# Kernel optimization log

Hardware: AMD Instinct MI355X
Metric: run time of the kernel (lower is better)

The kernel has to match this reference:

```python
import jax, jax.numpy as jnp
import numpy as np

B = 64          # batch
T = 12000       # signal length
P = 50          # patch size
D = 200         # embed dim
L = 12          # depth
H = 10          # heads
HD = D // H     # head dim = 20
FF = 4 * D      # mlp hidden = 800
N = T // P      # 240 patches
S = N + 1       # seq len with cls token
NRD = (2 * N - 1) * 1 + 3   # 482 relative distances (window (240,1))
NC = 1000       # classes
SCALE = HD ** -0.5
EPS = 1e-6


def _rel_index():
    # static [S,S] int index into the relative-position-bias table (window (N,1))
    w0, w1 = N, 1
    coords = np.stack(np.meshgrid(np.arange(w0), np.arange(w1), indexing='ij'))
    cf = coords.reshape(2, -1)                      # [2, N]
    rc = (cf[:, :, None] - cf[:, None, :]).transpose(1, 2, 0).copy()
    rc[:, :, 0] += w0 - 1
    rc[:, :, 1] += w1 - 1
    rc[:, :, 0] *= 2 * w1 - 1
    idx = np.zeros((w0 * w1 + 1,) * 2, dtype=np.int32)
    idx[1:, 1:] = rc.sum(-1)
    idx[0, :] = NRD - 3
    idx[:, 0] = NRD - 2
    idx[0, 0] = NRD - 1
    return idx

REL_IDX = jnp.asarray(_rel_index())


def _ln(x, s, b):
    m = x.mean(-1, keepdims=True)
    v = ((x - m) ** 2).mean(-1, keepdims=True)
    return (x - m) * jax.lax.rsqrt(v + EPS) * s + b


def setup_inputs() -> dict:
    key = jax.random.key(0)
    ks = jax.random.split(key, 12)
    nrm = lambda k, shp, std=0.02: jax.random.normal(k, shp, jnp.float32) * std
    return {
        'x': jax.random.normal(ks[0], (B, 1, T), jnp.float32),
        'conv_w': nrm(ks[1], (D, 1, P)),
        'conv_b': jnp.zeros((D,), jnp.float32),
        'cls_token': nrm(ks[2], (1, 1, D)),
        'pos_embed': nrm(ks[3], (1, S, D)),
        'ln1_s': jnp.ones((L, D), jnp.float32), 'ln1_b': jnp.zeros((L, D), jnp.float32),
        'qkv_w': nrm(ks[4], (L, 3 * D, D)),
        'q_bias': jnp.zeros((L, D), jnp.float32), 'v_bias': jnp.zeros((L, D), jnp.float32),
        'rpb_table': nrm(ks[5], (L, NRD, H)),
        'proj_w': nrm(ks[6], (L, D, D)), 'proj_b': jnp.zeros((L, D), jnp.float32),
        'ln2_s': jnp.ones((L, D), jnp.float32), 'ln2_b': jnp.zeros((L, D), jnp.float32),
        'fc1_w': nrm(ks[7], (L, FF, D)), 'fc1_b': jnp.zeros((L, FF), jnp.float32),
        'fc2_w': nrm(ks[8], (L, D, FF)), 'fc2_b': jnp.zeros((L, D), jnp.float32),
        'fc_norm_s': jnp.ones((D,), jnp.float32), 'fc_norm_b': jnp.zeros((D,), jnp.float32),
        'head_w': nrm(ks[9], (NC, D)), 'head_b': jnp.zeros((NC,), jnp.float32),
    }


def reference(x, conv_w, conv_b, cls_token, pos_embed,
              ln1_s, ln1_b, qkv_w, q_bias, v_bias, rpb_table, proj_w, proj_b,
              ln2_s, ln2_b, fc1_w, fc1_b, fc2_w, fc2_b,
              fc_norm_s, fc_norm_b, head_w, head_b):
    b = x.shape[0]
    # PatchEmbed: Conv1d with stride == kernel -> reshape + GEMM
    patches = x[:, 0].reshape(b, N, P)                       # [B,N,P]
    tok = patches @ conv_w[:, 0].T + conv_b                   # [B,N,D]
    tok = jnp.concatenate([jnp.broadcast_to(cls_token, (b, 1, D)), tok], axis=1)
    tok = tok + pos_embed                                     # [B,S,D]

    for i in range(L):
        h = _ln(tok, ln1_s[i], ln1_b[i])
        qkv_bias = jnp.concatenate([q_bias[i], jnp.zeros_like(v_bias[i]), v_bias[i]])
        qkv = (h @ qkv_w[i].T + qkv_bias).reshape(b, S, 3, H, HD)
        qkv = qkv.transpose(2, 0, 3, 1, 4)                    # [3,B,H,S,HD]
        q, k, v = qkv[0], qkv[1], qkv[2]
        attn = jnp.einsum('bhqd,bhkd->bhqk', q * SCALE, k)    # [B,H,S,S]
        bias = rpb_table[i][REL_IDX]                          # [S,S,H]
        attn = jax.nn.softmax(attn + bias.transpose(2, 0, 1)[None], axis=-1)
        o = jnp.einsum('bhqk,bhkd->bqhd', attn, v).reshape(b, S, D)
        tok = tok + o @ proj_w[i].T + proj_b[i]
        h2 = _ln(tok, ln2_s[i], ln2_b[i])
        h2 = jax.nn.gelu(h2 @ fc1_w[i].T + fc1_b[i], approximate=False)
        tok = tok + h2 @ fc2_w[i].T + fc2_b[i]

    pooled = _ln(tok[:, 1:].mean(axis=1), fc_norm_s, fc_norm_b)   # mean pooling over patch tokens
    return pooled @ head_w.T + head_b                             # [B, NC]
```

## Files before the change

### kernel.cpp

```cpp
#include <hip/hip_runtime.h>
#include <math.h>

#define Bz 64
#define Tz 12000
#define Pz 50
#define Dz 200
#define Lz 12
#define Hz 10
#define HDz 20
#define FFz 800
#define Nz 240
#define Sz 241
#define Sp 256
#define NRDz 482
#define NCz 1000
#define BS (Bz * Sz)
#define Mp (Bz * Sp)
#define Kp 224
#define PEM (Bz * Nz)
#define SCALEq 0.22360679774997896f
#define LOG2E 1.4426950408889634f
#define SCALE2f (SCALEq * LOG2E)
#define BIASL 655360

typedef __attribute__((ext_vector_type(8))) short bf16x8;
typedef __attribute__((ext_vector_type(4))) float f32x4;

static __device__ __forceinline__ short f2b(float f) {
    unsigned u = __float_as_uint(f);
    unsigned r = (u + 0x7fffu + ((u >> 16) & 1u)) >> 16;
    return (short)r;
}
static __device__ __forceinline__ float b2f(short v) {
    return __uint_as_float(((unsigned)(unsigned short)v) << 16);
}
static __device__ __forceinline__ uint2 pk4(float a, float b, float c, float d) {
    uint2 r;
    asm("v_cvt_pk_bf16_f32 %0, %1, %2" : "=v"(r.x) : "v"(a), "v"(b));
    asm("v_cvt_pk_bf16_f32 %0, %1, %2" : "=v"(r.y) : "v"(c), "v"(d));
    return r;
}
static __device__ __forceinline__ float frcp(float x) {
    float r;
    asm("v_rcp_f32 %0, %1" : "=v"(r) : "v"(x));
    return r;
}
static __device__ __forceinline__ float gelu_f(float v) {
    float u = v * (0.7978845608f + 0.03567740814f * v * v);
    float e = exp2f(2.885390082f * u);
    return v * e * frcp(e + 1.f);
}
static __device__ __forceinline__ void gll16(const void* g, void* l) {
    __builtin_amdgcn_global_load_lds((const __attribute__((address_space(1))) unsigned*)g,
                                     (__attribute__((address_space(3))) unsigned*)l, 16, 0, 0);
}
template <int N> static __device__ __forceinline__ void wait_vm() {
    if constexpr (N == 0) asm volatile("s_waitcnt vmcnt(0)" ::: "memory");
    else if constexpr (N == 1) asm volatile("s_waitcnt vmcnt(1)" ::: "memory");
    else if constexpr (N == 2) asm volatile("s_waitcnt vmcnt(2)" ::: "memory");
    else if constexpr (N == 3) asm volatile("s_waitcnt vmcnt(3)" ::: "memory");
    else if constexpr (N == 4) asm volatile("s_waitcnt vmcnt(4)" ::: "memory");
    else if constexpr (N == 5) asm volatile("s_waitcnt vmcnt(5)" ::: "memory");
    else if constexpr (N == 6) asm volatile("s_waitcnt vmcnt(6)" ::: "memory");
}

__global__ void cvt_pad_k(const float* __restrict__ in, short* __restrict__ out,
                          int N, int K, int Npad, int Kpad, int total) {
    int i = blockIdx.x * 256 + threadIdx.x;
    if (i >= total) return;
    int pk = Npad * Kpad;
    int l = i / pk;
    int r = i - l * pk;
    int n = r / Kpad;
    int k = r - n * Kpad;
    float v = (n < N && k < K) ? in[((size_t)l * N + n) * K + k] : 0.f;
    out[i] = f2b(v);
}

__global__ void xcvt_k(const float* __restrict__ x, short* __restrict__ xb) {
    int i = blockIdx.x * 256 + threadIdx.x;
    int m = i >> 6, k = i & 63;
    int b = m / Nz, j = m - b * Nz;
    xb[i] = (k < Pz) ? f2b(x[(size_t)b * Tz + j * Pz + k]) : 0;
}

__global__ void cls_k(const float* __restrict__ cls, const float* __restrict__ pos,
                      float* __restrict__ tok) {
    int b = blockIdx.x, d = threadIdx.x;
    if (d < Dz) tok[(size_t)b * Sp * Dz + d] = cls[d] + pos[d];
}

__global__ void ln_k(const float* __restrict__ in, short* __restrict__ out,
                     const float* __restrict__ sc, const float* __restrict__ bi) {
    int wave = threadIdx.x >> 6, lane = threadIdx.x & 63;
    int row = blockIdx.x * 4 + wave;
    if ((row & 255) >= Sz) return;
    const float* x = in + (size_t)row * Dz;
    float v[4];
    float sum = 0.f;
    #pragma unroll
    for (int i = 0; i < 4; ++i) {
        int d = lane + 64 * i;
        v[i] = (d < Dz) ? x[d] : 0.f;
        sum += v[i];
    }
    #pragma unroll
    for (int off = 32; off; off >>= 1) sum += __shfl_xor(sum, off);
    float mean = sum * (1.f / Dz);
    float var = 0.f;
    #pragma unroll
    for (int i = 0; i < 4; ++i) {
        int d = lane + 64 * i;
        if (d < Dz) { float t = v[i] - mean; var += t * t; }
    }
    #pragma unroll
    for (int off = 32; off; off >>= 1) var += __shfl_xor(var, off);
    var *= (1.f / Dz);
    float rstd = rsqrtf(var + 1e-6f);
    short* o = out + (size_t)row * Kp;
    #pragma unroll
    for (int i = 0; i < 4; ++i) {
        int d = lane + 64 * i;
        if (d < Dz) o[d] = f2b((v[i] - mean) * rstd * sc[d] + bi[d]);
        else if (d < Kp) o[d] = 0;
    }
}

__global__ void bias_pre4_k(const float* __restrict__ tabs, short* __restrict__ bp) {
    int l = blockIdx.y;
    int tid = blockIdx.x * 256 + threadIdx.x;
    const float* tab = tabs + (size_t)l * NRDz * Hz;
    int lane = tid & 63;
    int mi = (tid >> 6) & 1;
    int w  = (tid >> 7) & 3;
    int qb = (tid >> 9) & 1;
    int nj = (tid >> 10) & 3;
    int kc = (tid >> 12) & 3;
    int h  = tid >> 14;
    int q  = qb * 128 + w * 32 + mi * 16 + (lane & 15);
    int k0 = kc * 64 + nj * 16 + 4 * (lane >> 4);
    short4 o;
    #pragma unroll
    for (int r = 0; r < 4; ++r) {
        int k = k0 + r;
        float v;
        if (q > Nz || k > Nz) v = -1e30f;
        else if (k == 0)      v = (q == 0) ? tab[481 * Hz + h] : tab[480 * Hz + h];
        else if (q == 0)      v = tab[479 * Hz + h];
        else                  v = tab[(q - k + 239) * Hz + h];
        ((short*)&o)[r] = f2b(v * LOG2E);
    }
    *(short4*)(bp + (size_t)l * BIASL + (size_t)tid * 4) = o;
}

template <int MODE, int BN2, int BM2>
__global__ __launch_bounds__(256) void gemm8_k(
        const short* __restrict__ A, const short* __restrict__ W,
        const float* __restrict__ bias, const float* __restrict__ bias2,
        const float* __restrict__ res, void* __restrict__ outv,
        short* __restrict__ qo, short* __restrict__ ko, short* __restrict__ vo,
        int M, int Nreal, int K, int strideA, int ldo, int gridx, int gridy) {
    constexpr int NJ = BN2 / 32;
    constexpr int MI = BM2 / 32;
    constexpr int AISS = BM2 / 64;
    constexpr int BISS = BN2 / 64;
    constexpr int LPS = AISS + BISS;
    __shared__ short smem[3 * (BM2 + BN2) * 32];
    short* Asb = smem;
    short* Bsb = smem + 3 * BM2 * 32;
    const int t = threadIdx.x;
    const int lane = t & 63, w = t >> 6;
    const int l15 = lane & 15, lg = lane >> 4;
    const int wm = w & 1, wn = w >> 1;

    int bx, by;
    {
        int wg = blockIdx.x;
        if ((gridy & 7) == 0) {
            int xcd = wg & 7, j = wg >> 3;
            bx = j % gridx;
            by = (j / gridx) * 8 + xcd;
        } else {
            bx = wg % gridx;
            by = wg / gridx;
        }
    }
    const int row0 = by * BM2, col0 = bx * BN2;
    const int xsw = (l15 >> 1) & 3;

    f32x4 acc[MI][NJ];
    #pragma unroll
    for (int mi = 0; mi < MI; ++mi)
        #pragma unroll
        for (int nj = 0; nj < NJ; ++nj) {
            f32x4 z = {0.f, 0.f, 0.f, 0.f};
            acc[mi][nj] = z;
        }

    const int nk = K >> 5;

    auto stage = [&](int buf, int kt) {
        const int k0 = kt * 32;
        #pragma unroll
        for (int i = 0; i < AISS; ++i) {
            int c = (w * AISS + i) * 64 + lane;
            int r = c >> 2, q = c & 3;
            const short* gp = A + (size_t)(row0 + r) * strideA + k0 + ((q ^ ((r >> 1) & 3)) * 8);
            gll16(gp, Asb + buf * BM2 * 32 + (w * AISS + i) * 512);
        }
        #pragma unroll
        for (int i = 0; i < BISS; ++i) {
            int c = (w * BISS + i) * 64 + lane;
            int r = c >> 2, q = c & 3;
            const short* gp = W + (size_t)(col0 + r) * K + k0 + ((q ^ ((r >> 1) & 3)) * 8);
            gll16(gp, Bsb + buf * BN2 * 32 + (w * BISS + i) * 512);
        }
    };

    stage(0, 0);
    if (nk > 1) stage(1, 1);
    for (int kt = 0; kt < nk; ++kt) {
        const int cur = kt % 3;
        if (kt + 1 < nk) wait_vm<LPS>();
        else             wait_vm<0>();
        __builtin_amdgcn_s_barrier();
        if (kt + 2 < nk) stage((kt + 2) % 3, kt + 2);
        bf16x8 bfr[NJ], afr[MI];
        #pragma unroll
        for (int nj = 0; nj < NJ; ++nj)
            bfr[nj] = *(const bf16x8*)(Bsb + cur * BN2 * 32 + (wn * (BN2 / 2) + nj * 16 + l15) * 32 + ((lg ^ xsw) * 8));
        #pragma unroll
        for (int mi = 0; mi < MI; ++mi)
            afr[mi] = *(const bf16x8*)(Asb + cur * BM2 * 32 + (wm * (BM2 / 2) + mi * 16 + l15) * 32 + ((lg ^ xsw) * 8));
        #pragma unroll
        for (int mi = 0; mi < MI; ++mi)
            #pragma unroll
            for (int nj = 0; nj < NJ; ++nj) {
                if (MODE == 1)
                    acc[mi][nj] = __builtin_amdgcn_mfma_f32_16x16x32_bf16(bfr[nj], afr[mi], acc[mi][nj], 0, 0, 0);
                else
                    acc[mi][nj] = __builtin_amdgcn_mfma_f32_16x16x32_bf16(afr[mi], bfr[nj], acc[mi][nj], 0, 0, 0);
            }
    }

    if (MODE == 1) {
        #pragma unroll
        for (int mi = 0; mi < MI; ++mi) {
            int m = row0 + wm * (BM2 / 2) + mi * 16 + l15;
            int b = m >> 8, s = m & 255;
            #pragma unroll
            for (int nj = 0; nj < NJ; ++nj) {
                int n0 = col0 + wn * (BN2 / 2) + nj * 16 + 4 * lg;
                if (n0 >= 600) continue;
                int which = n0 >= 400 ? 2 : (n0 >= 200 ? 1 : 0);
                int hd = n0 - which * 200;
                int h = hd / 20, d0 = hd - h * 20;
                size_t base = (size_t)(b * Hz + h) * 8192;
                if (which == 0) {
                    f32x4 qb4 = *(const f32x4*)(bias + hd);
                    short4 o4;
                    #pragma unroll
                    for (int r = 0; r < 4; ++r)
                        ((short*)&o4)[r] = f2b((acc[mi][nj][r] + qb4[r]) * SCALE2f);
                    *(short4*)(qo + base + s * 32 + d0) = o4;
                } else if (which == 1) {
                    int oct = (d0 >> 3) ^ ((s >> 1) & 3);
                    short4 o4;
                    #pragma unroll
                    for (int r = 0; r < 4; ++r)
                        ((short*)&o4)[r] = f2b(acc[mi][nj][r]);
                    *(short4*)(ko + base + s * 32 + oct * 8 + (d0 & 7)) = o4;
                } else {
                    f32x4 vb4 = *(const f32x4*)(bias2 + hd);
                    #pragma unroll
                    for (int r = 0; r < 4; ++r) {
                        int d = d0 + r;
                        vo[base + d * 256 + (s ^ ((d & 7) << 3))] = f2b(acc[mi][nj][r] + vb4[r]);
                    }
                }
            }
        }
        return;
    }

    if (MODE == 2 || MODE == 3) {
        __syncthreads();
        if (MODE == 3) {
            constexpr int EW = BN2 + 8;
            short* ep = smem;
            #pragma unroll
            for (int mi = 0; mi < MI; ++mi)
                #pragma unroll
                for (int nj = 0; nj < NJ; ++nj) {
                    int nl = wn * (BN2 / 2) + nj * 16 + l15;
                    int n = col0 + nl;
                    float bv = (n < Nreal) ? bias[n] : 0.f;
                    #pragma unroll
                    for (int r = 0; r < 4; ++r)
                        ep[(wm * (BM2 / 2) + mi * 16 + 4 * lg + r) * EW + nl] =
                            f2b(gelu_f(acc[mi][nj][r] + bv));
                }
            __syncthreads();
            constexpr int TPR = BN2 / 8;
            constexpr int RPP = 256 / TPR;
            int rowp = t / TPR, cch = t % TPR;
            #pragma unroll
            for (int p = 0; p < BM2 / RPP; ++p) {
                int row = p * RPP + rowp;
                int n = col0 + cch * 8;
                if (n + 8 <= Nreal)
                    *(bf16x8*)((short*)outv + (size_t)(row0 + row) * ldo + n) =
                        *(const bf16x8*)(ep + row * EW + cch * 8);
            }
        } else {
            constexpr int EWF = BN2 + 4;
            float* epf = (float*)smem;
            #pragma unroll
            for (int mi = 0; mi < MI; ++mi)
                #pragma unroll
                for (int nj = 0; nj < NJ; ++nj) {
                    int nl = wn * (BN2 / 2) + nj * 16 + l15;
                    int n = col0 + nl;
                    float bv = (n < Nreal) ? bias[n] : 0.f;
                    #pragma unroll
                    for (int r = 0; r < 4; ++r)
                        epf[(wm * (BM2 / 2) + mi * 16 + 4 * lg + r) * EWF + nl] =
                            acc[mi][nj][r] + bv;
                }
            __syncthreads();
            constexpr int TPR = BN2 / 4;
            constexpr int RPP = 256 / TPR;
            int rowp = t / TPR, cch = t % TPR;
            #pragma unroll
            for (int p = 0; p < BM2 / RPP; ++p) {
                int row = p * RPP + rowp;
                int n = col0 + cch * 4;
                if (n + 4 <= Nreal) {
                    size_t off = (size_t)(row0 + row) * ldo + n;
                    f32x4 v = *(const f32x4*)(epf + row * EWF + cch * 4);
                    f32x4 rr = *(const f32x4*)(res + off);
                    *(f32x4*)((float*)outv + off) = v + rr;
                }
            }
        }
        return;
    }

    #pragma unroll
    for (int mi = 0; mi < MI; ++mi) {
        #pragma unroll
        for (int nj = 0; nj < NJ; ++nj) {
            int n = col0 + wn * (BN2 / 2) + nj * 16 + l15;
            if (n >= Nreal) continue;
            if (MODE == 4) {
                #pragma unroll
                for (int r = 0; r < 4; ++r) {
                    int m = row0 + wm * (BM2 / 2) + mi * 16 + 4 * lg + r;
                    int bb = m / Nz, j = m - bb * Nz;
                    size_t trow = (size_t)bb * Sp + j + 1;
                    ((float*)outv)[trow * ldo + n] =
                        acc[mi][nj][r] + bias[n] + res[(size_t)(j + 1) * Dz + n];
                }
            } else {
                #pragma unroll
                for (int r = 0; r < 4; ++r) {
                    int m = row0 + wm * (BM2 / 2) + mi * 16 + 4 * lg + r;
                    if (m >= M) continue;
                    size_t off = (size_t)m * ldo + n;
                    ((float*)outv)[off] = acc[mi][nj][r] + bias[n];
                }
            }
        }
    }
}

#define PLD 72
__global__ __launch_bounds__(256) void attn5_k(const short* __restrict__ Qb,
                                               const short* __restrict__ Kb,
                                               const short* __restrict__ Vtb,
                                               const short* __restrict__ biasC,
                                               short* __restrict__ o) {
    const int blk = blockIdx.x;
    const int qb = blk & 1;
    const int bh = blk >> 1;
    const int b = bh / Hz, h = bh - b * Hz;
    __shared__ short Ks[8192];
    __shared__ short Vt[8192];
    __shared__ short Pl[4][32 * PLD];
    const int t = threadIdx.x;
    const int lane = t & 63, w = t >> 6;
    const int l15 = lane & 15, lg = lane >> 4;

    const short* kbh = Kb + (size_t)bh * 8192;
    const short* vbh = Vtb + (size_t)bh * 8192;
    #pragma unroll
    for (int i = 0; i < 4; ++i) {
        int j = w * 4 + i;
        gll16(kbh + (size_t)(j * 64 + lane) * 8, Ks + j * 512);
        gll16(vbh + (size_t)(j * 64 + lane) * 8, Vt + j * 512);
    }
    bf16x8 qfrag[2];
    const short* qbh = Qb + (size_t)bh * 8192;
    #pragma unroll
    for (int mi = 0; mi < 2; ++mi) {
        int qrow = qb * 128 + w * 32 + mi * 16 + l15;
        qfrag[mi] = *(const bf16x8*)(qbh + qrow * 32 + lg * 8);
    }
    const short* bpp = biasC + 4 * (size_t)(lane + 128 * w + 512 * qb + 16384 * h);
    __syncthreads();

    f32x4 O[2][2];
    float mrow[2] = {-1e30f, -1e30f};
    float lrow[2] = {0.f, 0.f};
    {
        f32x4 z = {0.f, 0.f, 0.f, 0.f};
        O[0][0] = z; O[0][1] = z; O[1][0] = z; O[1][1] = z;
    }
    const int xsw = (l15 >> 1) & 3;

    #pragma unroll 1
    for (int kc = 0; kc < 4; ++kc) {
        bf16x8 kf[4];
        #pragma unroll
        for (int nj = 0; nj < 4; ++nj)
            kf[nj] = *(const bf16x8*)(Ks + (kc * 64 + nj * 16 + l15) * 32 + ((lg ^ xsw) * 8));
        f32x4 s[2][4];
        __builtin_amdgcn_s_setprio(1);
        #pragma unroll
        for (int mi = 0; mi < 2; ++mi)
            #pragma unroll
            for (int nj = 0; nj < 4; ++nj) {
                f32x4 z = {0.f, 0.f, 0.f, 0.f};
                s[mi][nj] = __builtin_amdgcn_mfma_f32_16x16x32_bf16(kf[nj], qfrag[mi], z, 0, 0, 0);
            }
        __builtin_amdgcn_s_setprio(0);
        const short* bkc = bpp + kc * 16384;
        #pragma unroll
        for (int mi = 0; mi < 2; ++mi)
            #pragma unroll
            for (int nj = 0; nj < 4; ++nj) {
                short4 bp4 = *(const short4*)(bkc + nj * 4096 + mi * 256);
                s[mi][nj][0] += b2f(bp4.x);
                s[mi][nj][1] += b2f(bp4.y);
                s[mi][nj][2] += b2f(bp4.z);
                s[mi][nj][3] += b2f(bp4.w);
            }
        #pragma unroll
        for (int mi = 0; mi < 2; ++mi) {
            float mx = s[mi][0][0];
            #pragma unroll
            for (int nj = 0; nj < 4; ++nj)
                #pragma unroll
                for (int c = 0; c < 4; ++c) mx = fmaxf(mx, s[mi][nj][c]);
            mx = fmaxf(mx, __shfl_xor(mx, 16));
            mx = fmaxf(mx, __shfl_xor(mx, 32));
            float ssum = 0.f;
            if (__all(mx - mrow[mi] <= 8.f)) {
                float mn = mrow[mi];
                #pragma unroll
                for (int nj = 0; nj < 4; ++nj)
                    #pragma unroll
                    for (int c = 0; c < 4; ++c) {
                        float p = exp2f(s[mi][nj][c] - mn);
                        s[mi][nj][c] = p;
                        ssum += p;
                    }
                ssum += __shfl_xor(ssum, 16);
                ssum += __shfl_xor(ssum, 32);
                lrow[mi] += ssum;
            } else {
                float mn = fmaxf(mrow[mi], mx);
                float scn = exp2f(mrow[mi] - mn);
                mrow[mi] = mn;
                #pragma unroll
                for (int nj = 0; nj < 4; ++nj)
                    #pragma unroll
                    for (int c = 0; c < 4; ++c) {
                        float p = exp2f(s[mi][nj][c] - mn);
                        s[mi][nj][c] = p;
                        ssum += p;
                    }
                ssum += __shfl_xor(ssum, 16);
                ssum += __shfl_xor(ssum, 32);
                lrow[mi] = lrow[mi] * scn + ssum;
                f32x4 scd;
                #pragma unroll
                for (int r = 0; r < 4; ++r) scd[r] = __shfl(scn, 4 * lg + r);
                O[mi][0] *= scd;
                O[mi][1] *= scd;
            }
            #pragma unroll
            for (int nj = 0; nj < 4; ++nj)
                *(uint2*)(Pl[w] + (mi * 16 + l15) * PLD + nj * 16 + 4 * lg) =
                    pk4(s[mi][nj][0], s[mi][nj][1], s[mi][nj][2], s[mi][nj][3]);
        }
        #pragma unroll
        for (int kk = 0; kk < 2; ++kk) {
            bf16x8 vf[2];
            #pragma unroll
            for (int dj = 0; dj < 2; ++dj) {
                int d = dj * 16 + l15;
                int cb = (kc * 128 + kk * 64 + lg * 16) ^ ((l15 & 7) << 4);
                vf[dj] = *(const bf16x8*)((const char*)Vt + d * 512 + cb);
            }
            __builtin_amdgcn_s_setprio(1);
            #pragma unroll
            for (int mi = 0; mi < 2; ++mi) {
                bf16x8 af = *(const bf16x8*)(Pl[w] + (mi * 16 + l15) * PLD + kk * 32 + lg * 8);
                O[mi][0] = __builtin_amdgcn_mfma_f32_16x16x32_bf16(af, vf[0], O[mi][0], 0, 0, 0);
                O[mi][1] = __builtin_amdgcn_mfma_f32_16x16x32_bf16(af, vf[1], O[mi][1], 0, 0, 0);
            }
            __builtin_amdgcn_s_setprio(0);
        }
    }

    #pragma unroll
    for (int mi = 0; mi < 2; ++mi) {
        float linv = 1.f / lrow[mi];
        f32x4 invd;
        #pragma unroll
        for (int r = 0; r < 4; ++r) invd[r] = __shfl(linv, 4 * lg + r);
        #pragma unroll
        for (int dj = 0; dj < 2; ++dj) {
            int d = dj * 16 + l15;
            if (d >= HDz) continue;
            #pragma unroll
            for (int r = 0; r < 4; ++r) {
                int q = qb * 128 + w * 32 + mi * 16 + 4 * lg + r;
                if (q < Sz)
                    o[((size_t)b * Sp + q) * Kp + h * HDz + d] = f2b(O[mi][dj][r] * invd[r]);
            }
        }
    }
}

__global__ void pool_norm_k(const float* __restrict__ tok, const float* __restrict__ sc,
                            const float* __restrict__ bi, short* __restrict__ pooled) {
    int b = blockIdx.x;
    int t = threadIdx.x;
    float val = 0.f;
    if (t < Dz) {
        const float* base = tok + ((size_t)b * Sp + 1) * Dz + t;
        float s = 0.f;
        for (int si = 0; si < Nz; ++si) s += base[(size_t)si * Dz];
        val = s * (1.f / Nz);
    }
    __shared__ float red[8];
    float sum = val, sq = val * val;
    #pragma unroll
    for (int off = 32; off; off >>= 1) { sum += __shfl_xor(sum, off); sq += __shfl_xor(sq, off); }
    int wave = t >> 6, lane = t & 63;
    if (lane == 0) { red[wave] = sum; red[4 + wave] = sq; }
    __syncthreads();
    sum = red[0] + red[1] + red[2] + red[3];
    sq = red[4] + red[5] + red[6] + red[7];
    float mean = sum * (1.f / Dz);
    float var = sq * (1.f / Dz) - mean * mean;
    float rstd = rsqrtf(var + 1e-6f);
    if (t < Dz) pooled[(size_t)b * Kp + t] = f2b((val - mean) * rstd * sc[t] + bi[t]);
    else if (t < Kp) pooled[(size_t)b * Kp + t] = 0;
}

extern "C" void kernel_launch(void* const* d_in, const int* in_sizes, int n_in,
                              void* d_out, int out_size, void* d_ws, size_t ws_size,
                              hipStream_t stream) {
    const float* x        = (const float*)d_in[0];
    const float* conv_w   = (const float*)d_in[1];
    const float* conv_b   = (const float*)d_in[2];
    const float* cls_tok  = (const float*)d_in[3];
    const float* pos_emb  = (const float*)d_in[4];
    const float* ln1_s    = (const float*)d_in[5];
    const float* ln1_b    = (const float*)d_in[6];
    const float* qkv_w    = (const float*)d_in[7];
    const float* q_bias   = (const float*)d_in[8];
    const float* v_bias   = (const float*)d_in[9];
    const float* rpb      = (const float*)d_in[10];
    const float* proj_w   = (const float*)d_in[11];
    const float* proj_b   = (const float*)d_in[12];
    const float* ln2_s    = (const float*)d_in[13];
    const float* ln2_b    = (const float*)d_in[14];
    const float* fc1_w    = (const float*)d_in[15];
    const float* fc1_b    = (const float*)d_in[16];
    const float* fc2_w    = (const float*)d_in[17];
    const float* fc2_b    = (const float*)d_in[18];
    const float* fcn_s    = (const float*)d_in[19];
    const float* fcn_b    = (const float*)d_in[20];
    const float* head_w   = (const float*)d_in[21];
    const float* head_b   = (const float*)d_in[22];
    float* out = (float*)d_out;

    char* ws = (char*)d_ws;
    float* tok  = (float*)ws;  ws += (size_t)Mp * Dz * 4;
    short* xa   = (short*)ws;  ws += (size_t)Mp * Kp * 2;
    short* xb   = (short*)ws;  ws += (size_t)Mp * Kp * 2;
    short* xc   = (short*)ws;  ws += (size_t)Mp * Kp * 2;
    short* mid  = (short*)ws;  ws += (size_t)Mp * FFz * 2;
    short* Qb   = (short*)ws;  ws += (size_t)640 * 8192 * 2;
    short* Kb   = (short*)ws;  ws += (size_t)640 * 8192 * 2;
    short* Vtb  = (short*)ws;  ws += (size_t)640 * 8192 * 2;
    short* wq = (short*)ws;    ws += (size_t)Lz * 640 * Kp * 2;
    short* wp = (short*)ws;    ws += (size_t)Lz * 256 * Kp * 2;
    short* w1 = (short*)ws;    ws += (size_t)Lz * 896 * Kp * 2;
    short* w2 = (short*)ws;    ws += (size_t)Lz * 256 * FFz * 2;
    short* wh = (short*)ws;    ws += (size_t)1024 * Kp * 2;
    short* biasC = (short*)ws; ws += (size_t)Lz * BIASL * 2;
    short* xpb  = (short*)ws;  ws += (size_t)PEM * 64 * 2;
    short* wpe  = (short*)ws;  ws += (size_t)256 * 64 * 2;
    short* pooledb = (short*)ws; ws += (size_t)128 * Kp * 2;

    hipMemsetAsync(xa, 0, (size_t)Mp * Kp * 2, stream);
    hipMemsetAsync(pooledb, 0, (size_t)128 * Kp * 2, stream);

    {
        int n;
        n = Lz * 640 * Kp;  cvt_pad_k<<<(n + 255) / 256, 256, 0, stream>>>(qkv_w, wq, 600, 200, 640, Kp, n);
        n = Lz * 256 * Kp;  cvt_pad_k<<<(n + 255) / 256, 256, 0, stream>>>(proj_w, wp, 200, 200, 256, Kp, n);
        n = Lz * 896 * Kp;  cvt_pad_k<<<(n + 255) / 256, 256, 0, stream>>>(fc1_w, w1, 800, 200, 896, Kp, n);
        n = Lz * 256 * FFz; cvt_pad_k<<<(n + 255) / 256, 256, 0, stream>>>(fc2_w, w2, 200, 800, 256, FFz, n);
        n = 1024 * Kp;      cvt_pad_k<<<(n + 255) / 256, 256, 0, stream>>>(head_w, wh, 1000, 200, 1024, Kp, n);
        n = 256 * 64;       cvt_pad_k<<<(n + 255) / 256, 256, 0, stream>>>(conv_w, wpe, 200, 50, 256, 64, n);
    }
    bias_pre4_k<<<dim3(640, Lz), 256, 0, stream>>>(rpb, biasC);

    xcvt_k<<<(PEM * 64) / 256, 256, 0, stream>>>(x, xpb);
    gemm8_k<4, 64, 128><<<4 * (PEM / 128), 256, 0, stream>>>(
        xpb, wpe, conv_b, nullptr, pos_emb, tok,
        nullptr, nullptr, nullptr, PEM, Dz, 64, 64, Dz, 4, PEM / 128);
    cls_k<<<Bz, 256, 0, stream>>>(cls_tok, pos_emb, tok);

    dim3 blk(256);
    ln_k<<<Mp / 4, blk, 0, stream>>>(tok, xa, ln1_s, ln1_b);
    for (int l = 0; l < Lz; ++l) {
        gemm8_k<1, 128, 64><<<5 * (Mp / 64), blk, 0, stream>>>(
            xa, wq + (size_t)l * 640 * Kp, q_bias + l * Dz, v_bias + l * Dz,
            nullptr, nullptr, Qb, Kb, Vtb,
            Mp, 600, Kp, Kp, 0, 5, Mp / 64);
        attn5_k<<<1280, blk, 0, stream>>>(Qb, Kb, Vtb, biasC + (size_t)l * BIASL, xb);
        gemm8_k<2, 64, 64><<<4 * (Mp / 64), blk, 0, stream>>>(
            xb, wp + (size_t)l * 256 * Kp, proj_b + l * Dz, nullptr,
            tok, tok, nullptr, nullptr, nullptr,
            Mp, Dz, Kp, Kp, Dz, 4, Mp / 64);
        ln_k<<<Mp / 4, blk, 0, stream>>>(tok, xc, ln2_s + l * Dz, ln2_b + l * Dz);
        gemm8_k<3, 128, 64><<<7 * (Mp / 64), blk, 0, stream>>>(
            xc, w1 + (size_t)l * 896 * Kp, fc1_b + l * FFz, nullptr,
            nullptr, mid, nullptr, nullptr, nullptr,
            Mp, FFz, Kp, Kp, FFz, 7, Mp / 64);
        gemm8_k<2, 64, 64><<<4 * (Mp / 64), blk, 0, stream>>>(
            mid, w2 + (size_t)l * 256 * FFz, fc2_b + l * Dz, nullptr,
            tok, tok, nullptr, nullptr, nullptr,
            Mp, Dz, FFz, FFz, Dz, 4, Mp / 64);
        ln_k<<<Mp / 4, blk, 0, stream>>>(tok, xa, ln1_s + (size_t)((l + 1) % Lz) * Dz,
                                         ln1_b + (size_t)((l + 1) % Lz) * Dz);
    }

    pool_norm_k<<<Bz, blk, 0, stream>>>(tok, fcn_s, fcn_b, pooledb);
    gemm8_k<0, 128, 128><<<8, blk, 0, stream>>>(
        pooledb, wh, head_b, nullptr, nullptr, out,
        nullptr, nullptr, nullptr, Bz, NCz, Kp, Kp, NCz, 8, 1);
}
```

Before: 1.355 ms.

## Process all query rows per (batch,head) block in attention; vectorize layernorm

The attention kernel now launches one block per (batch, head) instead of two, with each wave handling 64 query rows in two halves. This halves the redundant K/V loads into shared memory and is meant to reuse them across more queries. The bias precompute layout is changed to match the new indexing. LayerNorm switches to float4 loads and short4 stores. The cost is fewer blocks (640 on a large GPU), which lowers occupancy and parallelism, and more registers per wave.

```diff
diff --git a/kernel.cpp b/kernel.cpp
--- a/kernel.cpp
+++ b/kernel.cpp
@@ -96,48 +96,46 @@
     int row = blockIdx.x * 4 + wave;
     if ((row & 255) >= Sz) return;
     const float* x = in + (size_t)row * Dz;
-    float v[4];
-    float sum = 0.f;
-    #pragma unroll
-    for (int i = 0; i < 4; ++i) {
-        int d = lane + 64 * i;
-        v[i] = (d < Dz) ? x[d] : 0.f;
-        sum += v[i];
-    }
+    f32x4 v = {0.f, 0.f, 0.f, 0.f};
+    if (lane < 50) v = *(const f32x4*)(x + lane * 4);
+    float sum = v[0] + v[1] + v[2] + v[3];
     #pragma unroll
     for (int off = 32; off; off >>= 1) sum += __shfl_xor(sum, off);
     float mean = sum * (1.f / Dz);
     float var = 0.f;
-    #pragma unroll
-    for (int i = 0; i < 4; ++i) {
-        int d = lane + 64 * i;
-        if (d < Dz) { float t = v[i] - mean; var += t * t; }
+    if (lane < 50) {
+        #pragma unroll
+        for (int i = 0; i < 4; ++i) { float d = v[i] - mean; var += d * d; }
     }
     #pragma unroll
     for (int off = 32; off; off >>= 1) var += __shfl_xor(var, off);
-    var *= (1.f / Dz);
-    float rstd = rsqrtf(var + 1e-6f);
+    float rstd = rsqrtf(var * (1.f / Dz) + 1e-6f);
     short* o = out + (size_t)row * Kp;
-    #pragma unroll
-    for (int i = 0; i < 4; ++i) {
-        int d = lane + 64 * i;
-        if (d < Dz) o[d] = f2b((v[i] - mean) * rstd * sc[d] + bi[d]);
-        else if (d < Kp) o[d] = 0;
-    }
-}
-
-__global__ void bias_pre4_k(const float* __restrict__ tabs, short* __restrict__ bp) {
+    if (lane < 50) {
+        f32x4 s4 = *(const f32x4*)(sc + lane * 4);
+        f32x4 b4 = *(const f32x4*)(bi + lane * 4);
+        short4 o4;
+        #pragma unroll
+        for (int r = 0; r < 4; ++r)
+            ((short*)&o4)[r] = f2b((v[r] - mean) * rstd * s4[r] + b4[r]);
+        *(short4*)(o + lane * 4) = o4;
+    } else if (lane < 56) {
+        short4 z = {0, 0, 0, 0};
+        *(short4*)(o + lane * 4) = z;
+    }
+}
+
+__global__ void bias_pre5_k(const float* __restrict__ tabs, short* __restrict__ bp) {
     int l = blockIdx.y;
     int tid = blockIdx.x * 256 + threadIdx.x;
     const float* tab = tabs + (size_t)l * NRDz * Hz;
     int lane = tid & 63;
-    int mi = (tid >> 6) & 1;
-    int w  = (tid >> 7) & 3;
-    int qb = (tid >> 9) & 1;
+    int mi = (tid >> 6) & 3;
+    int w  = (tid >> 8) & 3;
     int nj = (tid >> 10) & 3;
     int kc = (tid >> 12) & 3;
     int h  = tid >> 14;
-    int q  = qb * 128 + w * 32 + mi * 16 + (lane & 15);
+    int q  = w * 64 + mi * 16 + (lane & 15);
     int k0 = kc * 64 + nj * 16 + 4 * (lane >> 4);
     short4 o;
     #pragma unroll
@@ -375,14 +373,12 @@
 }
 
 #define PLD 72
-__global__ __launch_bounds__(256) void attn5_k(const short* __restrict__ Qb,
+__global__ __launch_bounds__(256) void attn6_k(const short* __restrict__ Qb,
                                                const short* __restrict__ Kb,
                                                const short* __restrict__ Vtb,
                                                const short* __restrict__ biasC,
                                                short* __restrict__ o) {
-    const int blk = blockIdx.x;
-    const int qb = blk & 1;
-    const int bh = blk >> 1;
+    const int bh = blockIdx.x;
     const int b = bh / Hz, h = bh - b * Hz;
     __shared__ short Ks[8192];
     __shared__ short Vt[8192];
@@ -399,22 +395,23 @@
         gll16(kbh + (size_t)(j * 64 + lane) * 8, Ks + j * 512);
         gll16(vbh + (size_t)(j * 64 + lane) * 8, Vt + j * 512);
     }
-    bf16x8 qfrag[2];
+    bf16x8 qfrag[4];
     const short* qbh = Qb + (size_t)bh * 8192;
     #pragma unroll
-    for (int mi = 0; mi < 2; ++mi) {
-        int qrow = qb * 128 + w * 32 + mi * 16 + l15;
+    for (int mi = 0; mi < 4; ++mi) {
+        int qrow = w * 64 + mi * 16 + l15;
         qfrag[mi] = *(const bf16x8*)(qbh + qrow * 32 + lg * 8);
     }
-    const short* bpp = biasC + 4 * (size_t)(lane + 128 * w + 512 * qb + 16384 * h);
+    const short* bpp = biasC + 4 * (size_t)(lane + 256 * w + 16384 * h);
     __syncthreads();
 
-    f32x4 O[2][2];
-    float mrow[2] = {-1e30f, -1e30f};
-    float lrow[2] = {0.f, 0.f};
+    f32x4 O[4][2];
+    float mrow[4] = {-1e30f, -1e30f, -1e30f, -1e30f};
+    float lrow[4] = {0.f, 0.f, 0.f, 0.f};
     {
         f32x4 z = {0.f, 0.f, 0.f, 0.f};
-        O[0][0] = z; O[0][1] = z; O[1][0] = z; O[1][1] = z;
+        #pragma unroll
+        for (int mi = 0; mi < 4; ++mi) { O[mi][0] = z; O[mi][1] = z; }
     }
     const int xsw = (l15 >> 1) & 3;
 
@@ -424,98 +421,106 @@
         #pragma unroll
         for (int nj = 0; nj < 4; ++nj)
             kf[nj] = *(const bf16x8*)(Ks + (kc * 64 + nj * 16 + l15) * 32 + ((lg ^ xsw) * 8));
-        f32x4 s[2][4];
-        __builtin_amdgcn_s_setprio(1);
-        #pragma unroll
-        for (int mi = 0; mi < 2; ++mi)
-            #pragma unroll
-            for (int nj = 0; nj < 4; ++nj) {
-                f32x4 z = {0.f, 0.f, 0.f, 0.f};
-                s[mi][nj] = __builtin_amdgcn_mfma_f32_16x16x32_bf16(kf[nj], qfrag[mi], z, 0, 0, 0);
-            }
-        __builtin_amdgcn_s_setprio(0);
-        const short* bkc = bpp + kc * 16384;
-        #pragma unroll
-        for (int mi = 0; mi < 2; ++mi)
-            #pragma unroll
-            for (int nj = 0; nj < 4; ++nj) {
-                short4 bp4 = *(const short4*)(bkc + nj * 4096 + mi * 256);
-                s[mi][nj][0] += b2f(bp4.x);
-                s[mi][nj][1] += b2f(bp4.y);
-                s[mi][nj][2] += b2f(bp4.z);
-                s[mi][nj][3] += b2f(bp4.w);
-            }
-        #pragma unroll
-        for (int mi = 0; mi < 2; ++mi) {
-            float mx = s[mi][0][0];
-            #pragma unroll
-            for (int nj = 0; nj < 4; ++nj)
-                #pragma unroll
-                for (int c = 0; c < 4; ++c) mx = fmaxf(mx, s[mi][nj][c]);
-            mx = fmaxf(mx, __shfl_xor(mx, 16));
-            mx = fmaxf(mx, __shfl_xor(mx, 32));
-            float ssum = 0.f;
-            if (__all(mx - mrow[mi] <= 8.f)) {
-                float mn = mrow[mi];
+        #pragma unroll
+        for (int mih = 0; mih < 2; ++mih) {
+            f32x4 s[2][4];
+            __builtin_amdgcn_s_setprio(1);
+            #pragma unroll
+            for (int m2 = 0; m2 < 2; ++m2) {
+                int mi = mih * 2 + m2;
+                #pragma unroll
+                for (int nj = 0; nj < 4; ++nj) {
+                    f32x4 z = {0.f, 0.f, 0.f, 0.f};
+                    s[m2][nj] = __builtin_amdgcn_mfma_f32_16x16x32_bf16(kf[nj], qfrag[mi], z, 0, 0, 0);
+                }
+            }
+            __builtin_amdgcn_s_setprio(0);
+            #pragma unroll
+            for (int m2 = 0; m2 < 2; ++m2) {
+                int mi = mih * 2 + m2;
+                #pragma unroll
+                for (int nj = 0; nj < 4; ++nj) {
+                    short4 bp4 = *(const short4*)(bpp + 4 * (64 * mi + 1024 * nj + 4096 * kc));
+                    s[m2][nj][0] += b2f(bp4.x);
+                    s[m2][nj][1] += b2f(bp4.y);
+                    s[m2][nj][2] += b2f(bp4.z);
+                    s[m2][nj][3] += b2f(bp4.w);
+                }
+            }
+            #pragma unroll
+            for (int m2 = 0; m2 < 2; ++m2) {
+                int mi = mih * 2 + m2;
+                float mx = s[m2][0][0];
                 #pragma unroll
                 for (int nj = 0; nj < 4; ++nj)
                     #pragma unroll
-                    for (int c = 0; c < 4; ++c) {
-                        float p = exp2f(s[mi][nj][c] - mn);
-                        s[mi][nj][c] = p;
-                        ssum += p;
-                    }
-                ssum += __shfl_xor(ssum, 16);
-                ssum += __shfl_xor(ssum, 32);
-                lrow[mi] += ssum;
-            } else {
-                float mn = fmaxf(mrow[mi], mx);
-                float scn = exp2f(mrow[mi] - mn);
-                mrow[mi] = mn;
+                    for (int c = 0; c < 4; ++c) mx = fmaxf(mx, s[m2][nj][c]);
+                mx = fmaxf(mx, __shfl_xor(mx, 16));
+                mx = fmaxf(mx, __shfl_xor(mx, 32));
+                float ssum = 0.f;
+                if (__all(mx - mrow[mi] <= 8.f)) {
+                    float mn = mrow[mi];
+                    #pragma unroll
+                    for (int nj = 0; nj < 4; ++nj)
+                        #pragma unroll
+                        for (int c = 0; c < 4; ++c) {
+                            float p = exp2f(s[m2][nj][c] - mn);
+                            s[m2][nj][c] = p;
+                            ssum += p;
+                        }
+                    ssum += __shfl_xor(ssum, 16);
+                    ssum += __shfl_xor(ssum, 32);
+                    lrow[mi] += ssum;
+                } else {
+                    float mn = fmaxf(mrow[mi], mx);
+                    float scn = exp2f(mrow[mi] - mn);
+                    mrow[mi] = mn;
+                    #pragma unroll
+                    for (int nj = 0; nj < 4; ++nj)
+                        #pragma unroll
+                        for (int c = 0; c < 4; ++c) {
+                            float p = exp2f(s[m2][nj][c] - mn);
+                            s[m2][nj][c] = p;
+                            ssum += p;
+                        }
+                    ssum += __shfl_xor(ssum, 16);
+                    ssum += __shfl_xor(ssum, 32);
+                    lrow[mi] = lrow[mi] * scn + ssum;
+                    f32x4 scd;
+                    #pragma unroll
+                    for (int r = 0; r < 4; ++r) scd[r] = __shfl(scn, 4 * lg + r);
+                    O[mi][0] *= scd;
+                    O[mi][1] *= scd;
+                }
                 #pragma unroll
                 for (int nj = 0; nj < 4; ++nj)
-                    #pragma unroll
-                    for (int c = 0; c < 4; ++c) {
-                        float p = exp2f(s[mi][nj][c] - mn);
-                        s[mi][nj][c] = p;
-                        ssum += p;
-                    }
-                ssum += __shfl_xor(ssum, 16);
-                ssum += __shfl_xor(ssum, 32);
-                lrow[mi] = lrow[mi] * scn + ssum;
-                f32x4 scd;
-                #pragma unroll
-                for (int r = 0; r < 4; ++r) scd[r] = __shfl(scn, 4 * lg + r);
-                O[mi][0] *= scd;
-                O[mi][1] *= scd;
-            }
-            #pragma unroll
-            for (int nj = 0; nj < 4; ++nj)
-                *(uint2*)(Pl[w] + (mi * 16 + l15) * PLD + nj * 16 + 4 * lg) =
-                    pk4(s[mi][nj][0], s[mi][nj][1], s[mi][nj][2], s[mi][nj][3]);
-        }
-        #pragma unroll
-        for (int kk = 0; kk < 2; ++kk) {
-            bf16x8 vf[2];
-            #pragma unroll
-            for (int dj = 0; dj < 2; ++dj) {
-                int d = dj * 16 + l15;
-                int cb = (kc * 128 + kk * 64 + lg * 16) ^ ((l15 & 7) << 4);
-                vf[dj] = *(const bf16x8*)((const char*)Vt + d * 512 + cb);
-            }
-            __builtin_amdgcn_s_setprio(1);
-            #pragma unroll
-            for (int mi = 0; mi < 2; ++mi) {
-                bf16x8 af = *(const bf16x8*)(Pl[w] + (mi * 16 + l15) * PLD + kk * 32 + lg * 8);
-                O[mi][0] = __builtin_amdgcn_mfma_f32_16x16x32_bf16(af, vf[0], O[mi][0], 0, 0, 0);
-                O[mi][1] = __builtin_amdgcn_mfma_f32_16x16x32_bf16(af, vf[1], O[mi][1], 0, 0, 0);
-            }
-            __builtin_amdgcn_s_setprio(0);
-        }
-    }
-
-    #pragma unroll
-    for (int mi = 0; mi < 2; ++mi) {
+                    *(uint2*)(Pl[w] + (m2 * 16 + l15) * PLD + nj * 16 + 4 * lg) =
+                        pk4(s[m2][nj][0], s[m2][nj][1], s[m2][nj][2], s[m2][nj][3]);
+            }
+            #pragma unroll
+            for (int kk = 0; kk < 2; ++kk) {
+                bf16x8 vf[2];
+                #pragma unroll
+                for (int dj = 0; dj < 2; ++dj) {
+                    int d = dj * 16 + l15;
+                    int cb = (kc * 128 + kk * 64 + lg * 16) ^ ((l15 & 7) << 4);
+                    vf[dj] = *(const bf16x8*)((const char*)Vt + d * 512 + cb);
+                }
+                __builtin_amdgcn_s_setprio(1);
+                #pragma unroll
+                for (int m2 = 0; m2 < 2; ++m2) {
+                    int mi = mih * 2 + m2;
+                    bf16x8 af = *(const bf16x8*)(Pl[w] + (m2 * 16 + l15) * PLD + kk * 32 + lg * 8);
+                    O[mi][0] = __builtin_amdgcn_mfma_f32_16x16x32_bf16(af, vf[0], O[mi][0], 0, 0, 0);
+                    O[mi][1] = __builtin_amdgcn_mfma_f32_16x16x32_bf16(af, vf[1], O[mi][1], 0, 0, 0);
+                }
+                __builtin_amdgcn_s_setprio(0);
+            }
+        }
+    }
+
+    #pragma unroll
+    for (int mi = 0; mi < 4; ++mi) {
         float linv = 1.f / lrow[mi];
         f32x4 invd;
         #pragma unroll
@@ -526,7 +531,7 @@
             if (d >= HDz) continue;
             #pragma unroll
             for (int r = 0; r < 4; ++r) {
-                int q = qb * 128 + w * 32 + mi * 16 + 4 * lg + r;
+                int q = w * 64 + mi * 16 + 4 * lg + r;
                 if (q < Sz)
                     o[((size_t)b * Sp + q) * Kp + h * HDz + d] = f2b(O[mi][dj][r] * invd[r]);
             }
@@ -620,7 +625,7 @@
         n = 1024 * Kp;      cvt_pad_k<<<(n + 255) / 256, 256, 0, stream>>>(head_w, wh, 1000, 200, 1024, Kp, n);
         n = 256 * 64;       cvt_pad_k<<<(n + 255) / 256, 256, 0, stream>>>(conv_w, wpe, 200, 50, 256, 64, n);
     }
-    bias_pre4_k<<<dim3(640, Lz), 256, 0, stream>>>(rpb, biasC);
+    bias_pre5_k<<<dim3(640, Lz), 256, 0, stream>>>(rpb, biasC);
 
     xcvt_k<<<(PEM * 64) / 256, 256, 0, stream>>>(x, xpb);
     gemm8_k<4, 64, 128><<<4 * (PEM / 128), 256, 0, stream>>>(
@@ -635,7 +640,7 @@
             xa, wq + (size_t)l * 640 * Kp, q_bias + l * Dz, v_bias + l * Dz,
             nullptr, nullptr, Qb, Kb, Vtb,
             Mp, 600, Kp, Kp, 0, 5, Mp / 64);
-        attn5_k<<<1280, blk, 0, stream>>>(Qb, Kb, Vtb, biasC + (size_t)l * BIASL, xb);
+        attn6_k<<<640, blk, 0, stream>>>(Qb, Kb, Vtb, biasC + (size_t)l * BIASL, xb);
         gemm8_k<2, 64, 64><<<4 * (Mp / 64), blk, 0, stream>>>(
             xb, wp + (size_t)l * 256 * Kp, proj_b + l * Dz, nullptr,
             tok, tok, nullptr, nullptr, nullptr,
```

Measured after the change: 1.452 ms. +7.2%, slower.
